# Kernel tuning notes

Measured on AMD Instinct MI355X. Metric: run time of the kernel, lower is better.

## Reference

```python
import jax, jax.numpy as jnp
import numpy as np

V, E, D = 100000, 128, 60  # vocab, embedding_size, d_alpha
B, J, M, P = 512, 101, 50, 5120
EPS = 1e-6


def setup_inputs() -> dict:
    key = jax.random.key(0)
    ks = jax.random.split(key, 12)
    s = 0.5 / E
    inp = {
        'batch_titems': jax.random.randint(ks[0], (B, J), 0, V),
        'batch_citems': jax.random.randint(ks[1], (B, M), 0, V),
        'batch_pad_ids': jax.random.randint(ks[2], (2, P), 0, M),
        't_emb': jax.random.uniform(ks[3], (V, E), jnp.float32, -s, s),
        'c_emb': jax.random.uniform(ks[4], (V, E), jnp.float32, -s, s),
        'Ac_w': jax.random.normal(ks[5], (D, E), jnp.float32) * 0.05,
        'Ac_b': jnp.zeros((D,), jnp.float32),
        'At_w': jax.random.normal(ks[6], (D, E), jnp.float32) * 0.05,
        'At_b': jnp.zeros((D,), jnp.float32),
        'Bc_w': jax.random.normal(ks[7], (E, E), jnp.float32) * 0.05,
        'Bc_b': jnp.zeros((E,), jnp.float32),
        'R_w': jax.random.normal(ks[8], (E, E), jnp.float32) * 0.05,
        'R_b': jnp.zeros((E,), jnp.float32),
    }
    return inp


def reference(batch_titems, batch_citems, batch_pad_ids, t_emb, c_emb,
              Ac_w, Ac_b, At_w, At_b, Bc_w, Bc_b, R_w, R_b):
    v = t_emb[batch_titems]            # [B, J, E] target item vectors
    u = c_emb[batch_citems]            # [B, M, E] context item vectors
    tp = v @ At_w.T + At_b             # [B, J, D]
    cp = u @ Ac_w.T + Ac_b             # [B, M, D]
    # cosine similarity with torch eps clamp on norms
    dot = jnp.einsum('bjd,bmd->bjm', tp, cp)
    nt = jnp.maximum(jnp.linalg.norm(tp, axis=-1), EPS)  # [B, J]
    nc = jnp.maximum(jnp.linalg.norm(cp, axis=-1), EPS)  # [B, M]
    cos = dot / (nt[:, :, None] * nc[:, None, :])        # [B, J, M]
    # pad mask: (batch, context-pos) pairs masked across all J target rows
    mask = jnp.zeros((cos.shape[0], cos.shape[2]), bool)
    mask = mask.at[batch_pad_ids[0], batch_pad_ids[1]].set(True)
    scores = jnp.where(mask[:, None, :], -jnp.inf, cos)
    attn = jax.nn.softmax(scores, axis=-1)               # [B, J, M]
    bu = u @ Bc_w.T + Bc_b                               # [B, M, E]
    alpha = jnp.einsum('bjm,bme->bje', attn, bu)         # [B, J, E]
    return alpha @ R_w.T + R_b                           # [B, J, E]
```

## Files before the change

### kernel.cpp

```cpp
#include <hip/hip_runtime.h>

typedef unsigned short u16;
typedef unsigned int   u32;
typedef short bf8 __attribute__((ext_vector_type(8)));
typedef float f4  __attribute__((ext_vector_type(4)));

#define NB   512
#define NJ   101
#define NM   50
#define NE   128
#define ND   60
#define NP   5120
#define NT   1024
#define EPSV 1e-6f

#define U_B    0
#define T_B    17408
#define C_B    33536
#define H_B    42752
#define NT2_B  61184
#define NC2_B  61632
#define MSK_B  61888
#define ARENA  62144

__device__ __forceinline__ u16 f2bh(float f) {
    return (u16)((__float_as_uint(f) + 0x8000u) >> 16);
}
__device__ __forceinline__ u32 pk2(float a, float b) {
    u32 ia = __float_as_uint(a) + 0x8000u;
    u32 ib = __float_as_uint(b) + 0x8000u;
    return (ia >> 16) | (ib & 0xFFFF0000u);
}
__device__ __forceinline__ bf8 pkfrag(float4 x, float4 y) {
    union { u32 u[4]; bf8 v; } r;
    r.u[0] = pk2(x.x, x.y); r.u[1] = pk2(x.z, x.w);
    r.u[2] = pk2(y.x, y.y); r.u[3] = pk2(y.z, y.w);
    return r.v;
}

__global__ __launch_bounds__(128) void w2_kernel(
    const float* __restrict__ Bc_w, const float* __restrict__ Bc_b,
    const float* __restrict__ R_w,  const float* __restrict__ R_b,
    const float* __restrict__ At_w, const float* __restrict__ Ac_w,
    u16* __restrict__ w2t, float* __restrict__ rb2,
    u16* __restrict__ atw, u16* __restrict__ acw)
{
    const int e = blockIdx.x, k = threadIdx.x;
    const float* Rrow = R_w + e * NE;
    float a0 = 0.f, a1 = 0.f, a2 = 0.f, a3 = 0.f;
    #pragma unroll 8
    for (int j = 0; j < NE; j += 4) {
        a0 += Rrow[j]     * Bc_w[j * NE + k];
        a1 += Rrow[j + 1] * Bc_w[(j + 1) * NE + k];
        a2 += Rrow[j + 2] * Bc_w[(j + 2) * NE + k];
        a3 += Rrow[j + 3] * Bc_w[(j + 3) * NE + k];
    }
    w2t[e * NE + k] = f2bh((a0 + a1) + (a2 + a3));
    if (e < ND) {
        atw[e * NE + k] = f2bh(At_w[e * NE + k]);
        acw[e * NE + k] = f2bh(Ac_w[e * NE + k]);
    }
    float c = Bc_b[k] * Rrow[k];
    for (int o = 32; o; o >>= 1) c += __shfl_xor(c, o, 64);
    __shared__ float part[2];
    if ((k & 63) == 0) part[k >> 6] = c;
    __syncthreads();
    if (k == 0) rb2[e] = part[0] + part[1] + R_b[e];
}

__device__ __forceinline__ void ht_unit(int h, int l15, int quad,
    const u16* __restrict__ us16, const u16* __restrict__ w2t,
    u16* __restrict__ hT16)
{
    const int et = h >> 2, mt = h & 3;
    const u16* wrow = w2t + (size_t)(et * 16 + l15) * NE;
    bf8 U[4];
    #pragma unroll
    for (int ks = 0; ks < 4; ks++)
        U[ks] = *(const bf8*)(us16 + (mt * 16 + l15) * 136 + ks * 32 + quad * 8);
    f4 acc = {0.f, 0.f, 0.f, 0.f};
    #pragma unroll
    for (int ks = 0; ks < 4; ks++)
        acc = __builtin_amdgcn_mfma_f32_16x16x32_bf16(
            *(const bf8*)(wrow + ks * 32 + quad * 8), U[ks], acc, 0, 0, 0);
    const int e0 = et * 16 + quad * 4;
    #pragma unroll
    for (int r = 0; r < 4; r++)
        hT16[(e0 + r) * 72 + mt * 16 + l15] = f2bh(acc[r]);
}

__global__ __launch_bounds__(NT, 8) void aitv_kernel(
    const int* __restrict__ titems, const int* __restrict__ citems,
    const int* __restrict__ pad_ids,
    const float* __restrict__ t_emb, const float* __restrict__ c_emb,
    const u16* __restrict__ atw,     const float* __restrict__ At_b,
    const u16* __restrict__ acw,     const float* __restrict__ Ac_b,
    const u16* __restrict__ w2t,     const float* __restrict__ rb2g,
    float* __restrict__ out)
{
    const int b    = blockIdx.x;
    const int t    = threadIdx.x;
    const int wid  = t >> 6;
    const int lane = t & 63;
    const int l15  = lane & 15;
    const int quad = lane >> 4;

    __shared__ __align__(16) char arena[ARENA];
    u16*   us16 = (u16*)(arena + U_B);   u32* us32 = (u32*)(arena + U_B);
    u16*   tp16 = (u16*)(arena + T_B);   u16* at16 = (u16*)(arena + T_B);
    u16*   cp16 = (u16*)(arena + C_B);
    u16*   hT16 = (u16*)(arena + H_B);
    float* nt2  = (float*)(arena + NT2_B);
    float* nc2  = (float*)(arena + NC2_B);
    int*   msk  = (int*)(arena + MSK_B);

    float4 px[8];
    const int jt_w = wid >> 1;
    if (wid < 14) {
        int j = jt_w * 16 + l15; if (j > NJ - 1) j = NJ - 1;
        const float* vrow = t_emb + (size_t)titems[b * NJ + j] * NE + quad * 8;
        #pragma unroll
        for (int ks = 0; ks < 4; ks++) {
            px[2 * ks]     = *(const float4*)(vrow + ks * 32);
            px[2 * ks + 1] = *(const float4*)(vrow + ks * 32 + 4);
        }
    }

    #pragma unroll
    for (int i = 0; i < 4; i++) {
        int row = wid + i * 16;
        u32 val = 0;
        if (row < NM) {
            int idx = citems[b * NM + row];
            float2 x = *(const float2*)(c_emb + (size_t)idx * NE + 2 * lane);
            val = pk2(x.x, x.y);
        }
        us32[row * 68 + lane] = val;
    }
    if (t < 112) nt2[t] = 0.f;
    else if (t < 176) nc2[t - 112] = 0.f;
    else if (t < 240) msk[t - 176] = 0;

    bf8 A[4];
    if (wid < 14) {
        #pragma unroll
        for (int ks = 0; ks < 4; ks++) A[ks] = pkfrag(px[2 * ks], px[2 * ks + 1]);
    }
    __syncthreads();

    for (int i = t; i < NP; i += NT)
        if (pad_ids[i] == b) msk[pad_ids[NP + i]] = 1;

    for (int g = wid; g < 36; g += 16) {
        if (g < 14) {
            const int jt = g >> 1;
            const int d0 = (g & 1) * 2;
            #pragma unroll
            for (int dt2 = 0; dt2 < 2; dt2++) {
                const int dt = d0 + dt2;
                const int d = dt * 16 + l15;
                const u16* arow = atw + (size_t)((d < ND) ? d : 0) * NE;
                float bv = (d < ND) ? At_b[d] : 0.f;
                f4 acc = {bv, bv, bv, bv};
                #pragma unroll
                for (int ks = 0; ks < 4; ks++)
                    acc = __builtin_amdgcn_mfma_f32_16x16x32_bf16(
                        A[ks], *(const bf8*)(arow + ks * 32 + quad * 8), acc, 0, 0, 0);
                const int j0 = jt * 16 + quad * 4;
                #pragma unroll
                for (int r = 0; r < 4; r++) {
                    float v = acc[r];
                    tp16[(j0 + r) * 72 + d] = (d < ND) ? f2bh(v) : (u16)0;
                    float q = (d < ND) ? v * v : 0.f;
                    q += __shfl_xor(q, 1, 64); q += __shfl_xor(q, 2, 64);
                    q += __shfl_xor(q, 4, 64); q += __shfl_xor(q, 8, 64);
                    if (l15 == 0) atomicAdd(&nt2[j0 + r], q);
                }
            }
        } else if (g < 22) {
            const int c  = g - 14;
            const int mt = c >> 1;
            const int d0 = (c & 1) * 2;
            bf8 U[4];
            #pragma unroll
            for (int ks = 0; ks < 4; ks++)
                U[ks] = *(const bf8*)(us16 + (mt * 16 + l15) * 136 + ks * 32 + quad * 8);
            #pragma unroll
            for (int dt2 = 0; dt2 < 2; dt2++) {
                const int dt = d0 + dt2;
                const int d = dt * 16 + l15;
                const u16* arow = acw + (size_t)((d < ND) ? d : 0) * NE;
                float bv = (d < ND) ? Ac_b[d] : 0.f;
                f4 acc = {bv, bv, bv, bv};
                #pragma unroll
                for (int ks = 0; ks < 4; ks++)
                    acc = __builtin_amdgcn_mfma_f32_16x16x32_bf16(
                        U[ks], *(const bf8*)(arow + ks * 32 + quad * 8), acc, 0, 0, 0);
                const int m0 = mt * 16 + quad * 4;
                #pragma unroll
                for (int r = 0; r < 4; r++) {
                    float v = acc[r];
                    cp16[(m0 + r) * 72 + d] = (d < ND) ? f2bh(v) : (u16)0;
                    float q = (d < ND) ? v * v : 0.f;
                    q += __shfl_xor(q, 1, 64); q += __shfl_xor(q, 2, 64);
                    q += __shfl_xor(q, 4, 64); q += __shfl_xor(q, 8, 64);
                    if (l15 == 0) atomicAdd(&nc2[m0 + r], q);
                }
            }
        } else {
            ht_unit(g - 22, l15, quad, us16, w2t, hT16);
        }
    }
    __syncthreads();

    if (wid >= 7) {
        #pragma unroll
        for (int k2 = 0; k2 < 2; k2++)
            ht_unit(14 + (wid - 7) * 2 + k2, l15, quad, us16, w2t, hT16);
    } else {
        const int jt = wid;
        f4 S[4];
        #pragma unroll
        for (int mt = 0; mt < 4; mt++) {
            f4 acc = {0.f, 0.f, 0.f, 0.f};
            #pragma unroll
            for (int ks = 0; ks < 2; ks++) {
                bf8 a  = *(const bf8*)(tp16 + (jt * 16 + l15) * 72 + ks * 32 + quad * 8);
                bf8 bb = *(const bf8*)(cp16 + (mt * 16 + l15) * 72 + ks * 32 + quad * 8);
                acc = __builtin_amdgcn_mfma_f32_16x16x32_bf16(a, bb, acc, 0, 0, 0);
            }
            S[mt] = acc;
        }
        bool valid[4]; float ncS[4];
        #pragma unroll
        for (int mt = 0; mt < 4; mt++) {
            int m = mt * 16 + l15;
            valid[mt] = (m < NM) && (msk[m] == 0);
            ncS[mt]   = valid[mt] ? fmaxf(sqrtf(nc2[m]), EPSV) : 1.f;
        }
        #pragma unroll
        for (int r = 0; r < 4; r++) {
            int j = jt * 16 + quad * 4 + r;
            float ntj = fmaxf(sqrtf(nt2[j]), EPSV);
            float x[4], mx = -INFINITY;
            #pragma unroll
            for (int mt = 0; mt < 4; mt++) {
                x[mt] = valid[mt] ? S[mt][r] / (ntj * ncS[mt]) : -INFINITY;
                mx = fmaxf(mx, x[mt]);
            }
            mx = fmaxf(mx, __shfl_xor(mx, 1, 64)); mx = fmaxf(mx, __shfl_xor(mx, 2, 64));
            mx = fmaxf(mx, __shfl_xor(mx, 4, 64)); mx = fmaxf(mx, __shfl_xor(mx, 8, 64));
            float p[4], sm = 0.f;
            #pragma unroll
            for (int mt = 0; mt < 4; mt++) {
                p[mt] = valid[mt] ? __expf(x[mt] - mx) : 0.f;
                sm += p[mt];
            }
            sm += __shfl_xor(sm, 1, 64); sm += __shfl_xor(sm, 2, 64);
            sm += __shfl_xor(sm, 4, 64); sm += __shfl_xor(sm, 8, 64);
            float inv = (sm > 0.f) ? 1.f / sm : 0.f;
            #pragma unroll
            for (int mt = 0; mt < 4; mt++)
                at16[j * 72 + mt * 16 + l15] = f2bh(p[mt] * inv);
        }
    }
    __syncthreads();

    for (int u = wid; u < 56; u += 16) {
        int jt = u >> 3, et = u & 7;
        float bv = rb2g[et * 16 + l15];
        f4 acc = {bv, bv, bv, bv};
        #pragma unroll
        for (int ks = 0; ks < 2; ks++) {
            bf8 a  = *(const bf8*)(at16 + (jt * 16 + l15) * 72 + ks * 32 + quad * 8);
            bf8 bb = *(const bf8*)(hT16 + (et * 16 + l15) * 72 + ks * 32 + quad * 8);
            acc = __builtin_amdgcn_mfma_f32_16x16x32_bf16(a, bb, acc, 0, 0, 0);
        }
        int e = et * 16 + l15, j0 = jt * 16 + quad * 4;
        #pragma unroll
        for (int r = 0; r < 4; r++) {
            int j = j0 + r;
            if (j < NJ) out[((size_t)b * NJ + j) * NE + e] = acc[r];
        }
    }
}

extern "C" void kernel_launch(void* const* d_in, const int* in_sizes, int n_in,
                              void* d_out, int out_size, void* d_ws, size_t ws_size,
                              hipStream_t stream) {
    const int*   titems  = (const int*)d_in[0];
    const int*   citems  = (const int*)d_in[1];
    const int*   pad_ids = (const int*)d_in[2];
    const float* t_emb   = (const float*)d_in[3];
    const float* c_emb   = (const float*)d_in[4];
    const float* Ac_w    = (const float*)d_in[5];
    const float* Ac_b    = (const float*)d_in[6];
    const float* At_w    = (const float*)d_in[7];
    const float* At_b    = (const float*)d_in[8];
    const float* Bc_w    = (const float*)d_in[9];
    const float* Bc_b    = (const float*)d_in[10];
    const float* R_w     = (const float*)d_in[11];
    const float* R_b     = (const float*)d_in[12];
    float* out = (float*)d_out;

    u16*   w2t = (u16*)d_ws;
    float* rb2 = (float*)((char*)d_ws + 32768);
    u16*   atw = (u16*)((char*)d_ws + 33280);
    u16*   acw = (u16*)((char*)d_ws + 48640);

    w2_kernel<<<NE, NE, 0, stream>>>(Bc_w, Bc_b, R_w, R_b, At_w, Ac_w,
                                     w2t, rb2, atw, acw);
    aitv_kernel<<<NB, NT, 0, stream>>>(titems, citems, pad_ids, t_emb, c_emb,
                                       atw, At_b, acw, Ac_b, w2t, rb2, out);
}
```

Measured before the change: 180.9 us.

## Halve block size, drop shared context staging, load embeddings straight into MFMA fragments

Shrinks the workgroup from 16 to 8 waves and removes the shared-memory staging buffer for context embeddings. Each wave now gathers its context rows directly into registers as bf16 MFMA fragments and reuses them for either the full Bc-projection group or the Ac-projection tile. Work is redistributed so that waves 0-3 compute hT, waves 4-7 compute cp, and waves 0-6 compute tp for all four d-tiles. This reduces LDS footprint and synchronisation, at the cost of fewer waves per block and more serial MFMA work per wave, plus duplicate context-row loads across the two wave groups.

```diff
diff --git a/kernel.cpp b/kernel.cpp
--- a/kernel.cpp
+++ b/kernel.cpp
@@ -11,17 +11,16 @@
 #define NE   128
 #define ND   60
 #define NP   5120
-#define NT   1024
+#define NT   512
 #define EPSV 1e-6f
 
-#define U_B    0
-#define T_B    17408
-#define C_B    33536
-#define H_B    42752
-#define NT2_B  61184
-#define NC2_B  61632
-#define MSK_B  61888
-#define ARENA  62144
+#define T_B    0
+#define C_B    16128
+#define H_B    25344
+#define NT2_B  43776
+#define NC2_B  44224
+#define MSK_B  44480
+#define ARENA  44736
 
 __device__ __forceinline__ u16 f2bh(float f) {
     return (u16)((__float_as_uint(f) + 0x8000u) >> 16);
@@ -68,28 +67,79 @@
     if (k == 0) rb2[e] = part[0] + part[1] + R_b[e];
 }
 
-__device__ __forceinline__ void ht_unit(int h, int l15, int quad,
-    const u16* __restrict__ us16, const u16* __restrict__ w2t,
-    u16* __restrict__ hT16)
-{
-    const int et = h >> 2, mt = h & 3;
-    const u16* wrow = w2t + (size_t)(et * 16 + l15) * NE;
-    bf8 U[4];
-    #pragma unroll
-    for (int ks = 0; ks < 4; ks++)
-        U[ks] = *(const bf8*)(us16 + (mt * 16 + l15) * 136 + ks * 32 + quad * 8);
-    f4 acc = {0.f, 0.f, 0.f, 0.f};
-    #pragma unroll
-    for (int ks = 0; ks < 4; ks++)
-        acc = __builtin_amdgcn_mfma_f32_16x16x32_bf16(
-            *(const bf8*)(wrow + ks * 32 + quad * 8), U[ks], acc, 0, 0, 0);
-    const int e0 = et * 16 + quad * 4;
-    #pragma unroll
-    for (int r = 0; r < 4; r++)
-        hT16[(e0 + r) * 72 + mt * 16 + l15] = f2bh(acc[r]);
-}
-
-__global__ __launch_bounds__(NT, 8) void aitv_kernel(
+__device__ __forceinline__ void tp_full(int jt, int l15, int quad, const bf8* A,
+    const u16* __restrict__ atw, const float* __restrict__ At_b,
+    u16* __restrict__ tp16, float* __restrict__ nt2)
+{
+    #pragma unroll
+    for (int dt = 0; dt < 4; dt++) {
+        const int d = dt * 16 + l15;
+        const u16* arow = atw + (size_t)((d < ND) ? d : 0) * NE;
+        float bv = (d < ND) ? At_b[d] : 0.f;
+        f4 acc = {bv, bv, bv, bv};
+        #pragma unroll
+        for (int ks = 0; ks < 4; ks++)
+            acc = __builtin_amdgcn_mfma_f32_16x16x32_bf16(
+                A[ks], *(const bf8*)(arow + ks * 32 + quad * 8), acc, 0, 0, 0);
+        const int j0 = jt * 16 + quad * 4;
+        #pragma unroll
+        for (int r = 0; r < 4; r++) {
+            float v = acc[r];
+            tp16[(j0 + r) * 72 + d] = (d < ND) ? f2bh(v) : (u16)0;
+            float q = (d < ND) ? v * v : 0.f;
+            q += __shfl_xor(q, 1, 64); q += __shfl_xor(q, 2, 64);
+            q += __shfl_xor(q, 4, 64); q += __shfl_xor(q, 8, 64);
+            if (l15 == 0) atomicAdd(&nt2[j0 + r], q);
+        }
+    }
+}
+
+__device__ __forceinline__ void cp_full(int mt, int l15, int quad, const bf8* Au,
+    const u16* __restrict__ acw, const float* __restrict__ Ac_b,
+    u16* __restrict__ cp16, float* __restrict__ nc2)
+{
+    #pragma unroll
+    for (int dt = 0; dt < 4; dt++) {
+        const int d = dt * 16 + l15;
+        const u16* arow = acw + (size_t)((d < ND) ? d : 0) * NE;
+        float bv = (d < ND) ? Ac_b[d] : 0.f;
+        f4 acc = {bv, bv, bv, bv};
+        #pragma unroll
+        for (int ks = 0; ks < 4; ks++)
+            acc = __builtin_amdgcn_mfma_f32_16x16x32_bf16(
+                Au[ks], *(const bf8*)(arow + ks * 32 + quad * 8), acc, 0, 0, 0);
+        const int m0 = mt * 16 + quad * 4;
+        #pragma unroll
+        for (int r = 0; r < 4; r++) {
+            float v = acc[r];
+            cp16[(m0 + r) * 72 + d] = (d < ND) ? f2bh(v) : (u16)0;
+            float q = (d < ND) ? v * v : 0.f;
+            q += __shfl_xor(q, 1, 64); q += __shfl_xor(q, 2, 64);
+            q += __shfl_xor(q, 4, 64); q += __shfl_xor(q, 8, 64);
+            if (l15 == 0) atomicAdd(&nc2[m0 + r], q);
+        }
+    }
+}
+
+__device__ __forceinline__ void ht_group(int mtg, int l15, int quad, const bf8* Au,
+    const u16* __restrict__ w2t, u16* __restrict__ hT16)
+{
+    #pragma unroll
+    for (int et = 0; et < 8; et++) {
+        const u16* wrow = w2t + (size_t)(et * 16 + l15) * NE;
+        f4 acc = {0.f, 0.f, 0.f, 0.f};
+        #pragma unroll
+        for (int ks = 0; ks < 4; ks++)
+            acc = __builtin_amdgcn_mfma_f32_16x16x32_bf16(
+                *(const bf8*)(wrow + ks * 32 + quad * 8), Au[ks], acc, 0, 0, 0);
+        const int e0 = et * 16 + quad * 4;
+        #pragma unroll
+        for (int r = 0; r < 4; r++)
+            hT16[(e0 + r) * 72 + mtg * 16 + l15] = f2bh(acc[r]);
+    }
+}
+
+__global__ __launch_bounds__(NT, 3) void aitv_kernel(
     const int* __restrict__ titems, const int* __restrict__ citems,
     const int* __restrict__ pad_ids,
     const float* __restrict__ t_emb, const float* __restrict__ c_emb,
@@ -106,7 +156,6 @@
     const int quad = lane >> 4;
 
     __shared__ __align__(16) char arena[ARENA];
-    u16*   us16 = (u16*)(arena + U_B);   u32* us32 = (u32*)(arena + U_B);
     u16*   tp16 = (u16*)(arena + T_B);   u16* at16 = (u16*)(arena + T_B);
     u16*   cp16 = (u16*)(arena + C_B);
     u16*   hT16 = (u16*)(arena + H_B);
@@ -114,110 +163,45 @@
     float* nc2  = (float*)(arena + NC2_B);
     int*   msk  = (int*)(arena + MSK_B);
 
-    float4 px[8];
-    const int jt_w = wid >> 1;
-    if (wid < 14) {
-        int j = jt_w * 16 + l15; if (j > NJ - 1) j = NJ - 1;
-        const float* vrow = t_emb + (size_t)titems[b * NJ + j] * NE + quad * 8;
-        #pragma unroll
-        for (int ks = 0; ks < 4; ks++) {
-            px[2 * ks]     = *(const float4*)(vrow + ks * 32);
-            px[2 * ks + 1] = *(const float4*)(vrow + ks * 32 + 4);
-        }
-    }
-
-    #pragma unroll
-    for (int i = 0; i < 4; i++) {
-        int row = wid + i * 16;
-        u32 val = 0;
-        if (row < NM) {
-            int idx = citems[b * NM + row];
-            float2 x = *(const float2*)(c_emb + (size_t)idx * NE + 2 * lane);
-            val = pk2(x.x, x.y);
-        }
-        us32[row * 68 + lane] = val;
-    }
+    float4 pxT[8];
+    if (wid < 7) {
+        int j = wid * 16 + l15; if (j > NJ - 1) j = NJ - 1;
+        const float* vr = t_emb + (size_t)titems[b * NJ + j] * NE + quad * 8;
+        #pragma unroll
+        for (int h = 0; h < 8; h++)
+            pxT[h] = *(const float4*)(vr + (h >> 1) * 32 + (h & 1) * 4);
+    }
+    const int mtu = (wid < 4) ? wid : wid - 4;
+    int mrow = mtu * 16 + l15; if (mrow > NM - 1) mrow = NM - 1;
+    const float* vrU = c_emb + (size_t)citems[b * NM + mrow] * NE + quad * 8;
+
     if (t < 112) nt2[t] = 0.f;
     else if (t < 176) nc2[t - 112] = 0.f;
     else if (t < 240) msk[t - 176] = 0;
-
-    bf8 A[4];
-    if (wid < 14) {
-        #pragma unroll
-        for (int ks = 0; ks < 4; ks++) A[ks] = pkfrag(px[2 * ks], px[2 * ks + 1]);
-    }
-    __syncthreads();
+    __syncthreads();
+
+    float4 pxU[8];
+    #pragma unroll
+    for (int h = 0; h < 8; h++)
+        pxU[h] = *(const float4*)(vrU + (h >> 1) * 32 + (h & 1) * 4);
 
     for (int i = t; i < NP; i += NT)
         if (pad_ids[i] == b) msk[pad_ids[NP + i]] = 1;
 
-    for (int g = wid; g < 36; g += 16) {
-        if (g < 14) {
-            const int jt = g >> 1;
-            const int d0 = (g & 1) * 2;
-            #pragma unroll
-            for (int dt2 = 0; dt2 < 2; dt2++) {
-                const int dt = d0 + dt2;
-                const int d = dt * 16 + l15;
-                const u16* arow = atw + (size_t)((d < ND) ? d : 0) * NE;
-                float bv = (d < ND) ? At_b[d] : 0.f;
-                f4 acc = {bv, bv, bv, bv};
-                #pragma unroll
-                for (int ks = 0; ks < 4; ks++)
-                    acc = __builtin_amdgcn_mfma_f32_16x16x32_bf16(
-                        A[ks], *(const bf8*)(arow + ks * 32 + quad * 8), acc, 0, 0, 0);
-                const int j0 = jt * 16 + quad * 4;
-                #pragma unroll
-                for (int r = 0; r < 4; r++) {
-                    float v = acc[r];
-                    tp16[(j0 + r) * 72 + d] = (d < ND) ? f2bh(v) : (u16)0;
-                    float q = (d < ND) ? v * v : 0.f;
-                    q += __shfl_xor(q, 1, 64); q += __shfl_xor(q, 2, 64);
-                    q += __shfl_xor(q, 4, 64); q += __shfl_xor(q, 8, 64);
-                    if (l15 == 0) atomicAdd(&nt2[j0 + r], q);
-                }
-            }
-        } else if (g < 22) {
-            const int c  = g - 14;
-            const int mt = c >> 1;
-            const int d0 = (c & 1) * 2;
-            bf8 U[4];
-            #pragma unroll
-            for (int ks = 0; ks < 4; ks++)
-                U[ks] = *(const bf8*)(us16 + (mt * 16 + l15) * 136 + ks * 32 + quad * 8);
-            #pragma unroll
-            for (int dt2 = 0; dt2 < 2; dt2++) {
-                const int dt = d0 + dt2;
-                const int d = dt * 16 + l15;
-                const u16* arow = acw + (size_t)((d < ND) ? d : 0) * NE;
-                float bv = (d < ND) ? Ac_b[d] : 0.f;
-                f4 acc = {bv, bv, bv, bv};
-                #pragma unroll
-                for (int ks = 0; ks < 4; ks++)
-                    acc = __builtin_amdgcn_mfma_f32_16x16x32_bf16(
-                        U[ks], *(const bf8*)(arow + ks * 32 + quad * 8), acc, 0, 0, 0);
-                const int m0 = mt * 16 + quad * 4;
-                #pragma unroll
-                for (int r = 0; r < 4; r++) {
-                    float v = acc[r];
-                    cp16[(m0 + r) * 72 + d] = (d < ND) ? f2bh(v) : (u16)0;
-                    float q = (d < ND) ? v * v : 0.f;
-                    q += __shfl_xor(q, 1, 64); q += __shfl_xor(q, 2, 64);
-                    q += __shfl_xor(q, 4, 64); q += __shfl_xor(q, 8, 64);
-                    if (l15 == 0) atomicAdd(&nc2[m0 + r], q);
-                }
-            }
-        } else {
-            ht_unit(g - 22, l15, quad, us16, w2t, hT16);
-        }
-    }
-    __syncthreads();
-
-    if (wid >= 7) {
-        #pragma unroll
-        for (int k2 = 0; k2 < 2; k2++)
-            ht_unit(14 + (wid - 7) * 2 + k2, l15, quad, us16, w2t, hT16);
-    } else {
+    bf8 At[4];
+    if (wid < 7) {
+        #pragma unroll
+        for (int ks = 0; ks < 4; ks++) At[ks] = pkfrag(pxT[2 * ks], pxT[2 * ks + 1]);
+        tp_full(wid, l15, quad, At, atw, At_b, tp16, nt2);
+    }
+    bf8 Au[4];
+    #pragma unroll
+    for (int ks = 0; ks < 4; ks++) Au[ks] = pkfrag(pxU[2 * ks], pxU[2 * ks + 1]);
+    if (wid < 4) ht_group(mtu, l15, quad, Au, w2t, hT16);
+    else         cp_full(mtu, l15, quad, Au, acw, Ac_b, cp16, nc2);
+    __syncthreads();
+
+    if (wid < 7) {
         const int jt = wid;
         f4 S[4];
         #pragma unroll
@@ -266,7 +250,7 @@
     }
     __syncthreads();
 
-    for (int u = wid; u < 56; u += 16) {
+    for (int u = wid; u < 56; u += 8) {
         int jt = u >> 3, et = u & 7;
         float bv = rb2g[et * 16 + l15];
         f4 acc = {bv, bv, bv, bv};
```

Result: faster. 172.2 us (-4.8%).
